# Kernel tuning notes

Hardware: AMD Instinct MI355X
Metric: run time of the kernel (lower is better)

## Reference

```python
import jax, jax.numpy as jnp
import numpy as np

O = 100000   # num objects
R = 1000000  # num triplets
D = 128      # per-slot feature dim (input_dim[0]=input_dim[1]=input_dim[2])
SUM_D = 3 * D  # MLP in/out width
H = 256      # hidden_dim


def setup_inputs() -> dict:
    key = jax.random.key(0)
    k1, k2, k3, k4, k5 = jax.random.split(key, 5)
    object_feats = jax.random.normal(k1, (O, D), dtype=jnp.float32)
    relation_feats = jax.random.normal(k2, (R, D), dtype=jnp.float32)
    triplet = jax.random.randint(k3, (R, 3), 0, O, dtype=jnp.int64)
    # MLP: Linear(SUM_D->H) + ReLU + Linear(H->SUM_D), kaiming-normal init
    W1 = jax.random.normal(k4, (SUM_D, H), dtype=jnp.float32) * np.sqrt(2.0 / SUM_D)
    b1 = jnp.zeros((H,), dtype=jnp.float32)
    W2 = jax.random.normal(k5, (H, SUM_D), dtype=jnp.float32) * np.sqrt(2.0 / H)
    b2 = jnp.zeros((SUM_D,), dtype=jnp.float32)
    return {
        "object_feats": object_feats,
        "relation_feats": relation_feats,
        "W1": W1, "b1": b1, "W2": W2, "b2": b2,
        "triplet": triplet,
        "triplet_len": R,
    }


def reference(object_feats, relation_feats, W1, b1, W2, b2, triplet, triplet_len):
    t = triplet[:triplet_len]                      # [R, 3]
    subs = t[:, 0]                                 # [R]
    objs = t[:, 1]                                 # [R]
    # gather subj/obj feats, concat with relation feats -> [R, 3D]
    gcn_feat = jnp.concatenate(
        [object_feats[subs], relation_feats, object_feats[objs]], axis=1)
    # 2-layer MLP
    h = jax.nn.relu(gcn_feat @ W1 + b1)            # [R, H]
    out = h @ W2 + b2                              # [R, 3D]
    sub_out = out[:, :D]
    rel_out = out[:, D:-D]
    obj_out = out[:, -D:]
    # scatter-add back to object nodes, then mean by degree, plus residual
    acc = jnp.zeros_like(object_feats)
    acc = acc.at[subs].add(sub_out).at[objs].add(obj_out)   # [O, D]
    one = jnp.ones((triplet_len,), dtype=object_feats.dtype)
    cnt = jnp.zeros((object_feats.shape[0],), dtype=object_feats.dtype)
    cnt = cnt.at[subs].add(one).at[objs].add(one)           # [O]
    output_feat = acc / jnp.clip(cnt, 1.0)[:, None] + object_feats
    return (output_feat, rel_out, triplet, triplet_len)
```

## Files before the change

### kernel.cpp

```cpp
#include <hip/hip_runtime.h>

#define O_N 100000
#define R_N 1000000
#define DIM 128
#define SD 384
#define HD 256
#define BR 64
#define OBJ8 (O_N * DIM / 8)
#define REL8 (R_N * DIM / 8)

typedef __attribute__((ext_vector_type(8))) short short8;
typedef __attribute__((ext_vector_type(4))) float f32x4;

static __device__ __forceinline__ unsigned short f2bf(float x) {
    union { float f; unsigned int u; } v; v.f = x;
    unsigned int r = v.u + 0x7FFFu + ((v.u >> 16) & 1u);
    return (unsigned short)(r >> 16);
}
static __device__ __forceinline__ unsigned long long pack4(f32x4 v) {
    return  (unsigned long long)f2bf(v.x)
         | ((unsigned long long)f2bf(v.y) << 16)
         | ((unsigned long long)f2bf(v.z) << 32)
         | ((unsigned long long)f2bf(v.w) << 48);
}

__global__ void prep_weights(const float* __restrict__ W1, const float* __restrict__ W2,
                             unsigned short* __restrict__ W1T, unsigned short* __restrict__ W2T) {
    int i = blockIdx.x * 256 + threadIdx.x;
    if (i < SD * HD) {
        int h = i / SD, k = i - h * SD;
        W1T[i] = f2bf(W1[k * HD + h]);
    } else {
        int j = i - SD * HD;
        int c = j / HD, k = j - c * HD;
        W2T[j] = f2bf(W2[k * SD + c]);
    }
}

__global__ void conv_bf16(const float* __restrict__ objF, const float* __restrict__ relF,
                          unsigned short* __restrict__ objBF, unsigned short* __restrict__ relBF) {
    long long i = (long long)blockIdx.x * 256 + threadIdx.x;
    if (i >= (long long)OBJ8 + REL8) return;
    const float* s; unsigned short* d;
    if (i < OBJ8) { s = objF + i * 8;           d = objBF + i * 8; }
    else          { long long j = i - OBJ8; s = relF + j * 8; d = relBF + j * 8; }
    f32x4 v0 = ((const f32x4*)s)[0];
    f32x4 v1 = ((const f32x4*)s)[1];
    unsigned long long* dd = (unsigned long long*)d;
    dd[0] = pack4(v0);
    dd[1] = pack4(v1);
}

__global__ void trip_cnt(const int* __restrict__ trip, float* __restrict__ tripOut,
                         float* __restrict__ lenOut, float* __restrict__ cnt,
                         const int* __restrict__ tlen) {
    int i = blockIdx.x * 256 + threadIdx.x;
    if (i < R_N) {
        int s = trip[3 * i], o = trip[3 * i + 1], t2 = trip[3 * i + 2];
        tripOut[3 * i]     = (float)s;
        tripOut[3 * i + 1] = (float)o;
        tripOut[3 * i + 2] = (float)t2;
        atomicAdd(&cnt[min(max(s, 0), O_N - 1)], 1.0f);
        atomicAdd(&cnt[min(max(o, 0), O_N - 1)], 1.0f);
        if (i == 0) lenOut[0] = (float)tlen[0];
    }
}

__global__ __launch_bounds__(256, 3)
void mlp_kernel(const unsigned short* __restrict__ objBF, const unsigned short* __restrict__ relBF,
                const unsigned short* __restrict__ W1T, const unsigned short* __restrict__ W2T,
                const float* __restrict__ b1, const float* __restrict__ b2,
                const int* __restrict__ trip,
                float* __restrict__ accB, float* __restrict__ relOut) {
    __shared__ __align__(16) unsigned char smem[49664];
    unsigned char* Xs = smem;
    unsigned char* Hs = smem;
    int* idxBuf = (int*)(smem + 49152);

    const int tid  = threadIdx.x;
    const int lane = tid & 63;
    const int w    = tid >> 6;
    const int r0   = blockIdx.x * BR;
    const int l15  = lane & 15;
    const int l4   = lane >> 4;

    if (tid < 2 * BR) {
        int rr = r0 + (tid & (BR - 1));
        int which = tid >> 6;
        idxBuf[tid] = min(max(trip[3 * rr + which], 0), O_N - 1);
    }
    __syncthreads();

    #pragma unroll
    for (int j = 0; j < 12; ++j) {
        int seg = w * 12 + j;
        int a   = seg * 64 + lane;
        int row = a / 48;
        int p   = a - row * 48;
        int u   = p ^ (row & 15);
        const unsigned short* src;
        if (u < 16)      src = objBF + (size_t)idxBuf[row] * DIM + u * 8;
        else if (u < 32) src = relBF + (size_t)(r0 + row) * DIM + (u - 16) * 8;
        else             src = objBF + (size_t)idxBuf[BR + row] * DIM + (u - 32) * 8;
        __builtin_amdgcn_global_load_lds(
            (const __attribute__((address_space(1))) void*)src,
            (__attribute__((address_space(3))) void*)(Xs + seg * 1024),
            16, 0, 0);
    }
    __syncthreads();

    const int hW = w * 64;
    f32x4 acc1[4][4];
    #pragma unroll
    for (int a = 0; a < 4; ++a)
        #pragma unroll
        for (int b = 0; b < 4; ++b) acc1[a][b] = (f32x4)0.0f;

    #pragma unroll
    for (int ks = 0; ks < 12; ++ks) {
        int k0 = ks * 32;
        short8 af[4], bfr[4];
        #pragma unroll
        for (int mh = 0; mh < 4; ++mh) {
            int h = hW + mh * 16 + l15;
            af[mh] = *(const short8*)(W1T + h * SD + k0 + 8 * l4);
        }
        #pragma unroll
        for (int nr = 0; nr < 4; ++nr) {
            int rel = nr * 16 + l15;
            int kb  = (k0 >> 3) + l4;
            bfr[nr] = *(const short8*)(Xs + rel * 768 + ((kb ^ (rel & 15)) << 4));
        }
        #pragma unroll
        for (int mh = 0; mh < 4; ++mh)
            #pragma unroll
            for (int nr = 0; nr < 4; ++nr)
                acc1[mh][nr] = __builtin_amdgcn_mfma_f32_16x16x32_bf16(
                    af[mh], bfr[nr], acc1[mh][nr], 0, 0, 0);
    }
    __syncthreads();

    #pragma unroll
    for (int mh = 0; mh < 4; ++mh) {
        int hbase = hW + mh * 16 + 4 * l4;
        float bb0 = b1[hbase], bb1 = b1[hbase + 1], bb2 = b1[hbase + 2], bb3 = b1[hbase + 3];
        int hb   = hbase >> 3;
        int half = (hbase >> 2) & 1;
        #pragma unroll
        for (int nr = 0; nr < 4; ++nr) {
            int rel = nr * 16 + l15;
            unsigned long long pk =
                  (unsigned long long)f2bf(fmaxf(acc1[mh][nr][0] + bb0, 0.f))
                | ((unsigned long long)f2bf(fmaxf(acc1[mh][nr][1] + bb1, 0.f)) << 16)
                | ((unsigned long long)f2bf(fmaxf(acc1[mh][nr][2] + bb2, 0.f)) << 32)
                | ((unsigned long long)f2bf(fmaxf(acc1[mh][nr][3] + bb3, 0.f)) << 48);
            *(unsigned long long*)(Hs + rel * 512 + ((hb ^ (rel & 15)) << 4) + half * 8) = pk;
        }
    }
    __syncthreads();

    const int cW = w * 96;
    f32x4 acc2[4][6];
    #pragma unroll
    for (int a = 0; a < 4; ++a)
        #pragma unroll
        for (int b = 0; b < 6; ++b) acc2[a][b] = (f32x4)0.0f;

    #pragma unroll
    for (int ks = 0; ks < 8; ++ks) {
        int k0 = ks * 32;
        short8 ha[4], wb[6];
        #pragma unroll
        for (int ma = 0; ma < 4; ++ma) {
            int rel = ma * 16 + l15;
            int hb  = (k0 >> 3) + l4;
            ha[ma] = *(const short8*)(Hs + rel * 512 + ((hb ^ (rel & 15)) << 4));
        }
        #pragma unroll
        for (int nb = 0; nb < 6; ++nb) {
            int c = cW + nb * 16 + l15;
            wb[nb] = *(const short8*)(W2T + c * HD + k0 + 8 * l4);
        }
        #pragma unroll
        for (int ma = 0; ma < 4; ++ma)
            #pragma unroll
            for (int nb = 0; nb < 6; ++nb)
                acc2[ma][nb] = __builtin_amdgcn_mfma_f32_16x16x32_bf16(
                    ha[ma], wb[nb], acc2[ma][nb], 0, 0, 0);
    }

    #pragma unroll
    for (int ma = 0; ma < 4; ++ma) {
        int rloc = ma * 16 + 4 * l4;
        int rg   = r0 + rloc;
        int subs[4], objs[4];
        #pragma unroll
        for (int q = 0; q < 4; ++q) {
            subs[q] = idxBuf[rloc + q];
            objs[q] = idxBuf[BR + rloc + q];
        }
        #pragma unroll
        for (int nb = 0; nb < 6; ++nb) {
            int c = cW + nb * 16 + l15;
            float b2v = b2[c];
            #pragma unroll
            for (int q = 0; q < 4; ++q) {
                float v = acc2[ma][nb][q] + b2v;
                if (c < DIM) {
                    atomicAdd(accB + (size_t)subs[q] * DIM + c, v);
                } else if (c < 2 * DIM) {
                    relOut[(size_t)(rg + q) * DIM + (c - DIM)] = v;
                } else {
                    atomicAdd(accB + (size_t)objs[q] * DIM + (c - 2 * DIM), v);
                }
            }
        }
    }
}

__global__ void finalize(const float* __restrict__ accB, const float* __restrict__ cnt,
                         const float* __restrict__ objF, float* __restrict__ outF) {
    int i = blockIdx.x * 256 + threadIdx.x;
    if (i < O_N * DIM / 4) {
        int row = i >> 5;
        float c = fmaxf(cnt[row], 1.0f);
        f32x4 a = ((const f32x4*)accB)[i];
        f32x4 o = ((const f32x4*)objF)[i];
        f32x4 r;
        r.x = a.x / c + o.x;
        r.y = a.y / c + o.y;
        r.z = a.z / c + o.z;
        r.w = a.w / c + o.w;
        ((f32x4*)outF)[i] = r;
    }
}

extern "C" void kernel_launch(void* const* d_in, const int* in_sizes, int n_in,
                              void* d_out, int out_size, void* d_ws, size_t ws_size,
                              hipStream_t stream) {
    const float* objF = (const float*)d_in[0];
    const float* relF = (const float*)d_in[1];
    const float* W1   = (const float*)d_in[2];
    const float* b1   = (const float*)d_in[3];
    const float* W2   = (const float*)d_in[4];
    const float* b2   = (const float*)d_in[5];
    const int*   trip = (const int*)d_in[6];
    const int*   tlen = (const int*)d_in[7];

    float* outF    = (float*)d_out;
    float* relOut  = outF + (size_t)O_N * DIM;
    float* tripOut = relOut + (size_t)R_N * DIM;
    float* lenOut  = tripOut + (size_t)R_N * 3;

    unsigned short* W1T = (unsigned short*)d_ws;
    unsigned short* W2T = W1T + SD * HD;
    float* accB = (float*)(W2T + SD * HD);
    float* cnt  = accB + (size_t)O_N * DIM;
    unsigned short* objBF = (unsigned short*)(cnt + O_N);
    unsigned short* relBF = objBF + (size_t)O_N * DIM;

    (void)hipMemsetAsync(accB, 0, ((size_t)O_N * DIM + O_N) * sizeof(float), stream);
    prep_weights<<<(2 * SD * HD) / 256, 256, 0, stream>>>(W1, W2, W1T, W2T);
    conv_bf16<<<(OBJ8 + REL8 + 255) / 256, 256, 0, stream>>>(objF, relF, objBF, relBF);
    trip_cnt<<<(R_N + 255) / 256, 256, 0, stream>>>(trip, tripOut, lenOut, cnt, tlen);
    mlp_kernel<<<R_N / BR, 256, 0, stream>>>(objBF, relBF, W1T, W2T, b1, b2, trip, accB, relOut);
    finalize<<<(O_N * DIM / 4 + 255) / 256, 256, 0, stream>>>(accB, cnt, objF, outF);
}
```

Before: 1.519 ms.

## Make MLP kernel persistent and prefetch next tile's gathered rows during compute

Converts the MLP kernel to a persistent grid of 512 blocks that loop over row tiles. It separates the X and H shared buffers so the next tile's gather into LDS can be issued while the second GEMM and the atomic scatter of the current tile run. The triplet kernel now writes clamped subject and object index arrays, so the MLP reads indices directly instead of staging them in LDS. This raises LDS use and lowers occupancy (launch bounds 3 to 2), and the hand-placed waitcnt and barrier synchronisation adds correctness risk.

```diff
diff --git a/kernel.cpp b/kernel.cpp
--- a/kernel.cpp
+++ b/kernel.cpp
@@ -6,11 +6,14 @@
 #define SD 384
 #define HD 256
 #define BR 64
+#define NT (R_N / BR)
+#define GRIDP 512
 #define OBJ8 (O_N * DIM / 8)
 #define REL8 (R_N * DIM / 8)
 
 typedef __attribute__((ext_vector_type(8))) short short8;
 typedef __attribute__((ext_vector_type(4))) float f32x4;
+typedef __attribute__((ext_vector_type(4))) int i32x4;
 
 static __device__ __forceinline__ unsigned short f2bf(float x) {
     union { float f; unsigned int u; } v; v.f = x;
@@ -53,6 +56,7 @@
 
 __global__ void trip_cnt(const int* __restrict__ trip, float* __restrict__ tripOut,
                          float* __restrict__ lenOut, float* __restrict__ cnt,
+                         int* __restrict__ subIdx, int* __restrict__ objIdx,
                          const int* __restrict__ tlen) {
     int i = blockIdx.x * 256 + threadIdx.x;
     if (i < R_N) {
@@ -60,162 +64,179 @@
         tripOut[3 * i]     = (float)s;
         tripOut[3 * i + 1] = (float)o;
         tripOut[3 * i + 2] = (float)t2;
-        atomicAdd(&cnt[min(max(s, 0), O_N - 1)], 1.0f);
-        atomicAdd(&cnt[min(max(o, 0), O_N - 1)], 1.0f);
+        int sc = min(max(s, 0), O_N - 1);
+        int oc = min(max(o, 0), O_N - 1);
+        subIdx[i] = sc;
+        objIdx[i] = oc;
+        atomicAdd(&cnt[sc], 1.0f);
+        atomicAdd(&cnt[oc], 1.0f);
         if (i == 0) lenOut[0] = (float)tlen[0];
     }
 }
 
-__global__ __launch_bounds__(256, 3)
+__global__ __launch_bounds__(256, 2)
 void mlp_kernel(const unsigned short* __restrict__ objBF, const unsigned short* __restrict__ relBF,
                 const unsigned short* __restrict__ W1T, const unsigned short* __restrict__ W2T,
                 const float* __restrict__ b1, const float* __restrict__ b2,
-                const int* __restrict__ trip,
+                const int* __restrict__ subIdx, const int* __restrict__ objIdx,
                 float* __restrict__ accB, float* __restrict__ relOut) {
-    __shared__ __align__(16) unsigned char smem[49664];
-    unsigned char* Xs = smem;
-    unsigned char* Hs = smem;
-    int* idxBuf = (int*)(smem + 49152);
+    __shared__ __align__(16) unsigned char Xs[49152];
+    __shared__ __align__(16) unsigned char Hs[32768];
 
     const int tid  = threadIdx.x;
     const int lane = tid & 63;
     const int w    = tid >> 6;
-    const int r0   = blockIdx.x * BR;
     const int l15  = lane & 15;
     const int l4   = lane >> 4;
-
-    if (tid < 2 * BR) {
-        int rr = r0 + (tid & (BR - 1));
-        int which = tid >> 6;
-        idxBuf[tid] = min(max(trip[3 * rr + which], 0), O_N - 1);
-    }
-    __syncthreads();
-
-    #pragma unroll
-    for (int j = 0; j < 12; ++j) {
-        int seg = w * 12 + j;
-        int a   = seg * 64 + lane;
-        int row = a / 48;
-        int p   = a - row * 48;
-        int u   = p ^ (row & 15);
-        const unsigned short* src;
-        if (u < 16)      src = objBF + (size_t)idxBuf[row] * DIM + u * 8;
-        else if (u < 32) src = relBF + (size_t)(r0 + row) * DIM + (u - 16) * 8;
-        else             src = objBF + (size_t)idxBuf[BR + row] * DIM + (u - 32) * 8;
-        __builtin_amdgcn_global_load_lds(
-            (const __attribute__((address_space(1))) void*)src,
-            (__attribute__((address_space(3))) void*)(Xs + seg * 1024),
-            16, 0, 0);
-    }
-    __syncthreads();
-
-    const int hW = w * 64;
-    f32x4 acc1[4][4];
-    #pragma unroll
-    for (int a = 0; a < 4; ++a)
-        #pragma unroll
-        for (int b = 0; b < 4; ++b) acc1[a][b] = (f32x4)0.0f;
-
-    #pragma unroll
-    for (int ks = 0; ks < 12; ++ks) {
-        int k0 = ks * 32;
-        short8 af[4], bfr[4];
+    const int hW   = w * 64;
+    const int cW   = w * 96;
+
+    #define FILL(TT)                                                          \
+    {                                                                         \
+        int rb_ = (TT) * BR;                                                  \
+        _Pragma("unroll")                                                     \
+        for (int j = 0; j < 12; ++j) {                                        \
+            int seg = w * 12 + j;                                             \
+            int a   = seg * 64 + lane;                                        \
+            int row = a / 48;                                                 \
+            int p   = a - row * 48;                                           \
+            int u   = p ^ (row & 15);                                         \
+            const unsigned short* src;                                        \
+            if (u < 16)      src = objBF + (size_t)subIdx[rb_ + row] * DIM + u * 8;        \
+            else if (u < 32) src = relBF + (size_t)(rb_ + row) * DIM + (u - 16) * 8;       \
+            else             src = objBF + (size_t)objIdx[rb_ + row] * DIM + (u - 32) * 8; \
+            __builtin_amdgcn_global_load_lds(                                 \
+                (const __attribute__((address_space(1))) void*)src,           \
+                (__attribute__((address_space(3))) void*)(Xs + seg * 1024),   \
+                16, 0, 0);                                                    \
+        }                                                                     \
+    }
+
+    int t = blockIdx.x;
+    if (t < NT) FILL(t);
+    asm volatile("s_waitcnt vmcnt(0)" ::: "memory");
+    __builtin_amdgcn_s_barrier();
+    __builtin_amdgcn_sched_barrier(0);
+
+    for (; t < NT; t += GRIDP) {
+        f32x4 acc1[4][4];
+        #pragma unroll
+        for (int a = 0; a < 4; ++a)
+            #pragma unroll
+            for (int b = 0; b < 4; ++b) acc1[a][b] = (f32x4)0.0f;
+
+        #pragma unroll
+        for (int ks = 0; ks < 12; ++ks) {
+            int k0 = ks * 32;
+            short8 af[4], bfr[4];
+            #pragma unroll
+            for (int mh = 0; mh < 4; ++mh) {
+                int h = hW + mh * 16 + l15;
+                af[mh] = *(const short8*)(W1T + h * SD + k0 + 8 * l4);
+            }
+            #pragma unroll
+            for (int nr = 0; nr < 4; ++nr) {
+                int rel = nr * 16 + l15;
+                int kb  = (k0 >> 3) + l4;
+                bfr[nr] = *(const short8*)(Xs + rel * 768 + ((kb ^ (rel & 15)) << 4));
+            }
+            #pragma unroll
+            for (int mh = 0; mh < 4; ++mh)
+                #pragma unroll
+                for (int nr = 0; nr < 4; ++nr)
+                    acc1[mh][nr] = __builtin_amdgcn_mfma_f32_16x16x32_bf16(
+                        af[mh], bfr[nr], acc1[mh][nr], 0, 0, 0);
+        }
+
+        __builtin_amdgcn_s_barrier();
+        __builtin_amdgcn_sched_barrier(0);
+
         #pragma unroll
         for (int mh = 0; mh < 4; ++mh) {
-            int h = hW + mh * 16 + l15;
-            af[mh] = *(const short8*)(W1T + h * SD + k0 + 8 * l4);
-        }
-        #pragma unroll
-        for (int nr = 0; nr < 4; ++nr) {
-            int rel = nr * 16 + l15;
-            int kb  = (k0 >> 3) + l4;
-            bfr[nr] = *(const short8*)(Xs + rel * 768 + ((kb ^ (rel & 15)) << 4));
-        }
-        #pragma unroll
-        for (int mh = 0; mh < 4; ++mh)
-            #pragma unroll
-            for (int nr = 0; nr < 4; ++nr)
-                acc1[mh][nr] = __builtin_amdgcn_mfma_f32_16x16x32_bf16(
-                    af[mh], bfr[nr], acc1[mh][nr], 0, 0, 0);
-    }
-    __syncthreads();
-
-    #pragma unroll
-    for (int mh = 0; mh < 4; ++mh) {
-        int hbase = hW + mh * 16 + 4 * l4;
-        float bb0 = b1[hbase], bb1 = b1[hbase + 1], bb2 = b1[hbase + 2], bb3 = b1[hbase + 3];
-        int hb   = hbase >> 3;
-        int half = (hbase >> 2) & 1;
-        #pragma unroll
-        for (int nr = 0; nr < 4; ++nr) {
-            int rel = nr * 16 + l15;
-            unsigned long long pk =
-                  (unsigned long long)f2bf(fmaxf(acc1[mh][nr][0] + bb0, 0.f))
-                | ((unsigned long long)f2bf(fmaxf(acc1[mh][nr][1] + bb1, 0.f)) << 16)
-                | ((unsigned long long)f2bf(fmaxf(acc1[mh][nr][2] + bb2, 0.f)) << 32)
-                | ((unsigned long long)f2bf(fmaxf(acc1[mh][nr][3] + bb3, 0.f)) << 48);
-            *(unsigned long long*)(Hs + rel * 512 + ((hb ^ (rel & 15)) << 4) + half * 8) = pk;
-        }
-    }
-    __syncthreads();
-
-    const int cW = w * 96;
-    f32x4 acc2[4][6];
-    #pragma unroll
-    for (int a = 0; a < 4; ++a)
-        #pragma unroll
-        for (int b = 0; b < 6; ++b) acc2[a][b] = (f32x4)0.0f;
-
-    #pragma unroll
-    for (int ks = 0; ks < 8; ++ks) {
-        int k0 = ks * 32;
-        short8 ha[4], wb[6];
-        #pragma unroll
-        for (int ma = 0; ma < 4; ++ma) {
-            int rel = ma * 16 + l15;
-            int hb  = (k0 >> 3) + l4;
-            ha[ma] = *(const short8*)(Hs + rel * 512 + ((hb ^ (rel & 15)) << 4));
-        }
-        #pragma unroll
-        for (int nb = 0; nb < 6; ++nb) {
-            int c = cW + nb * 16 + l15;
-            wb[nb] = *(const short8*)(W2T + c * HD + k0 + 8 * l4);
-        }
-        #pragma unroll
-        for (int ma = 0; ma < 4; ++ma)
-            #pragma unroll
-            for (int nb = 0; nb < 6; ++nb)
-                acc2[ma][nb] = __builtin_amdgcn_mfma_f32_16x16x32_bf16(
-                    ha[ma], wb[nb], acc2[ma][nb], 0, 0, 0);
-    }
-
-    #pragma unroll
-    for (int ma = 0; ma < 4; ++ma) {
-        int rloc = ma * 16 + 4 * l4;
-        int rg   = r0 + rloc;
-        int subs[4], objs[4];
-        #pragma unroll
-        for (int q = 0; q < 4; ++q) {
-            subs[q] = idxBuf[rloc + q];
-            objs[q] = idxBuf[BR + rloc + q];
-        }
-        #pragma unroll
-        for (int nb = 0; nb < 6; ++nb) {
-            int c = cW + nb * 16 + l15;
-            float b2v = b2[c];
-            #pragma unroll
-            for (int q = 0; q < 4; ++q) {
-                float v = acc2[ma][nb][q] + b2v;
-                if (c < DIM) {
-                    atomicAdd(accB + (size_t)subs[q] * DIM + c, v);
-                } else if (c < 2 * DIM) {
-                    relOut[(size_t)(rg + q) * DIM + (c - DIM)] = v;
-                } else {
-                    atomicAdd(accB + (size_t)objs[q] * DIM + (c - 2 * DIM), v);
+            int hbase = hW + mh * 16 + 4 * l4;
+            float bb0 = b1[hbase], bb1 = b1[hbase + 1], bb2 = b1[hbase + 2], bb3 = b1[hbase + 3];
+            int hb   = hbase >> 3;
+            int half = (hbase >> 2) & 1;
+            #pragma unroll
+            for (int nr = 0; nr < 4; ++nr) {
+                int rel = nr * 16 + l15;
+                unsigned long long pk =
+                      (unsigned long long)f2bf(fmaxf(acc1[mh][nr][0] + bb0, 0.f))
+                    | ((unsigned long long)f2bf(fmaxf(acc1[mh][nr][1] + bb1, 0.f)) << 16)
+                    | ((unsigned long long)f2bf(fmaxf(acc1[mh][nr][2] + bb2, 0.f)) << 32)
+                    | ((unsigned long long)f2bf(fmaxf(acc1[mh][nr][3] + bb3, 0.f)) << 48);
+                *(unsigned long long*)(Hs + rel * 512 + ((hb ^ (rel & 15)) << 4) + half * 8) = pk;
+            }
+        }
+        {
+            int tn = t + GRIDP;
+            if (tn < NT) FILL(tn);
+        }
+        asm volatile("s_waitcnt lgkmcnt(0)" ::: "memory");
+        __builtin_amdgcn_s_barrier();
+        __builtin_amdgcn_sched_barrier(0);
+
+        f32x4 acc2[4][6];
+        #pragma unroll
+        for (int a = 0; a < 4; ++a)
+            #pragma unroll
+            for (int b = 0; b < 6; ++b) acc2[a][b] = (f32x4)0.0f;
+
+        #pragma unroll
+        for (int ks = 0; ks < 8; ++ks) {
+            int k0 = ks * 32;
+            short8 ha[4], wb[6];
+            #pragma unroll
+            for (int ma = 0; ma < 4; ++ma) {
+                int rel = ma * 16 + l15;
+                int hb  = (k0 >> 3) + l4;
+                ha[ma] = *(const short8*)(Hs + rel * 512 + ((hb ^ (rel & 15)) << 4));
+            }
+            #pragma unroll
+            for (int nb = 0; nb < 6; ++nb) {
+                int c = cW + nb * 16 + l15;
+                wb[nb] = *(const short8*)(W2T + c * HD + k0 + 8 * l4);
+            }
+            #pragma unroll
+            for (int ma = 0; ma < 4; ++ma)
+                #pragma unroll
+                for (int nb = 0; nb < 6; ++nb)
+                    acc2[ma][nb] = __builtin_amdgcn_mfma_f32_16x16x32_bf16(
+                        ha[ma], wb[nb], acc2[ma][nb], 0, 0, 0);
+        }
+
+        asm volatile("s_waitcnt vmcnt(0)" ::: "memory");
+        __builtin_amdgcn_s_barrier();
+        __builtin_amdgcn_sched_barrier(0);
+
+        {
+            int r0t = t * BR;
+            #pragma unroll
+            for (int ma = 0; ma < 4; ++ma) {
+                int rloc = ma * 16 + 4 * l4;
+                int rg   = r0t + rloc;
+                i32x4 sv = *(const i32x4*)(subIdx + rg);
+                i32x4 ov = *(const i32x4*)(objIdx + rg);
+                #pragma unroll
+                for (int nb = 0; nb < 6; ++nb) {
+                    int c = cW + nb * 16 + l15;
+                    float b2v = b2[c];
+                    #pragma unroll
+                    for (int q = 0; q < 4; ++q) {
+                        float v = acc2[ma][nb][q] + b2v;
+                        if (c < DIM) {
+                            atomicAdd(accB + (size_t)sv[q] * DIM + c, v);
+                        } else if (c < 2 * DIM) {
+                            relOut[(size_t)(rg + q) * DIM + (c - DIM)] = v;
+                        } else {
+                            atomicAdd(accB + (size_t)ov[q] * DIM + (c - 2 * DIM), v);
+                        }
+                    }
                 }
             }
         }
     }
+    #undef FILL
 }
 
 __global__ void finalize(const float* __restrict__ accB, const float* __restrict__ cnt,
@@ -258,11 +279,13 @@
     float* cnt  = accB + (size_t)O_N * DIM;
     unsigned short* objBF = (unsigned short*)(cnt + O_N);
     unsigned short* relBF = objBF + (size_t)O_N * DIM;
+    int* subIdx = (int*)(relBF + (size_t)R_N * DIM);
+    int* objIdx = subIdx + R_N;
 
     (void)hipMemsetAsync(accB, 0, ((size_t)O_N * DIM + O_N) * sizeof(float), stream);
     prep_weights<<<(2 * SD * HD) / 256, 256, 0, stream>>>(W1, W2, W1T, W2T);
     conv_bf16<<<(OBJ8 + REL8 + 255) / 256, 256, 0, stream>>>(objF, relF, objBF, relBF);
-    trip_cnt<<<(R_N + 255) / 256, 256, 0, stream>>>(trip, tripOut, lenOut, cnt, tlen);
-    mlp_kernel<<<R_N / BR, 256, 0, stream>>>(objBF, relBF, W1T, W2T, b1, b2, trip, accB, relOut);
+    trip_cnt<<<(R_N + 255) / 256, 256, 0, stream>>>(trip, tripOut, lenOut, cnt, subIdx, objIdx, tlen);
+    mlp_kernel<<<GRIDP, 256, 0, stream>>>(objBF, relBF, W1T, W2T, b1, b2, subIdx, objIdx, accB, relOut);
     finalize<<<(O_N * DIM / 4 + 255) / 256, 256, 0, stream>>>(accB, cnt, objF, outF);
 }
```

After: 3.293 ms. 2.17x slower.

## Process two row tiles per block, prefetching the second tile during the epilogue

Applied to the files above, without the earlier changes.

Each block now handles two 64-row tiles, so half as many blocks are launched. After the second GEMM of the first tile, the block issues the asynchronous global-to-LDS gather for the second tile before running the atomic scatter epilogue, so the gather latency overlaps the epilogue. The second tile's indices are loaded while the first tile's hidden activations are being written. Halving the grid may reduce load balance and adds an extra barrier per tile.

```diff
diff --git a/kernel.cpp b/kernel.cpp
--- a/kernel.cpp
+++ b/kernel.cpp
@@ -6,6 +6,8 @@
 #define SD 384
 #define HD 256
 #define BR 64
+#define NT (R_N / BR)
+#define NB ((NT + 1) / 2)
 #define OBJ8 (O_N * DIM / 8)
 #define REL8 (R_N * DIM / 8)
 
@@ -72,150 +74,176 @@
                 const float* __restrict__ b1, const float* __restrict__ b2,
                 const int* __restrict__ trip,
                 float* __restrict__ accB, float* __restrict__ relOut) {
-    __shared__ __align__(16) unsigned char smem[49664];
+    __shared__ __align__(16) unsigned char smem[50176];
     unsigned char* Xs = smem;
     unsigned char* Hs = smem;
-    int* idxBuf = (int*)(smem + 49152);
+    int* idxA = (int*)(smem + 49152);
+    int* idxB = idxA + 128;
 
     const int tid  = threadIdx.x;
     const int lane = tid & 63;
     const int w    = tid >> 6;
-    const int r0   = blockIdx.x * BR;
     const int l15  = lane & 15;
     const int l4   = lane >> 4;
+    const int hW   = w * 64;
+    const int cW   = w * 96;
+
+    const int t1 = blockIdx.x;
+    const int t2 = blockIdx.x + NB;
+    const int hasT2 = (t2 < NT);
+
+    #define FILL(RB, IDXP)                                                    \
+    {                                                                         \
+        _Pragma("unroll")                                                     \
+        for (int j = 0; j < 12; ++j) {                                        \
+            int seg = w * 12 + j;                                             \
+            int a   = seg * 64 + lane;                                        \
+            int row = a / 48;                                                 \
+            int p   = a - row * 48;                                           \
+            int u   = p ^ (row & 15);                                         \
+            const unsigned short* src;                                        \
+            if (u < 16)      src = objBF + (size_t)(IDXP)[row] * DIM + u * 8;          \
+            else if (u < 32) src = relBF + (size_t)((RB) + row) * DIM + (u - 16) * 8;  \
+            else             src = objBF + (size_t)(IDXP)[BR + row] * DIM + (u - 32) * 8; \
+            __builtin_amdgcn_global_load_lds(                                 \
+                (const __attribute__((address_space(1))) void*)src,           \
+                (__attribute__((address_space(3))) void*)(Xs + seg * 1024),   \
+                16, 0, 0);                                                    \
+        }                                                                     \
+    }
 
     if (tid < 2 * BR) {
-        int rr = r0 + (tid & (BR - 1));
-        int which = tid >> 6;
-        idxBuf[tid] = min(max(trip[3 * rr + which], 0), O_N - 1);
+        int rr = t1 * BR + (tid & (BR - 1));
+        idxA[tid] = min(max(trip[3 * rr + (tid >> 6)], 0), O_N - 1);
     }
     __syncthreads();
-
-    #pragma unroll
-    for (int j = 0; j < 12; ++j) {
-        int seg = w * 12 + j;
-        int a   = seg * 64 + lane;
-        int row = a / 48;
-        int p   = a - row * 48;
-        int u   = p ^ (row & 15);
-        const unsigned short* src;
-        if (u < 16)      src = objBF + (size_t)idxBuf[row] * DIM + u * 8;
-        else if (u < 32) src = relBF + (size_t)(r0 + row) * DIM + (u - 16) * 8;
-        else             src = objBF + (size_t)idxBuf[BR + row] * DIM + (u - 32) * 8;
-        __builtin_amdgcn_global_load_lds(
-            (const __attribute__((address_space(1))) void*)src,
-            (__attribute__((address_space(3))) void*)(Xs + seg * 1024),
-            16, 0, 0);
-    }
-    __syncthreads();
-
-    const int hW = w * 64;
-    f32x4 acc1[4][4];
-    #pragma unroll
-    for (int a = 0; a < 4; ++a)
-        #pragma unroll
-        for (int b = 0; b < 4; ++b) acc1[a][b] = (f32x4)0.0f;
-
-    #pragma unroll
-    for (int ks = 0; ks < 12; ++ks) {
-        int k0 = ks * 32;
-        short8 af[4], bfr[4];
+    FILL(t1 * BR, idxA);
+
+    #pragma unroll 2
+    for (int s = 0; s < 2; ++s) {
+        if (s && !hasT2) break;
+        const int t = s ? t2 : t1;
+        const int* idxCur = s ? idxB : idxA;
+
+        __syncthreads();
+
+        f32x4 acc1[4][4];
+        #pragma unroll
+        for (int a = 0; a < 4; ++a)
+            #pragma unroll
+            for (int b = 0; b < 4; ++b) acc1[a][b] = (f32x4)0.0f;
+
+        #pragma unroll
+        for (int ks = 0; ks < 12; ++ks) {
+            int k0 = ks * 32;
+            short8 af[4], bfr[4];
+            #pragma unroll
+            for (int mh = 0; mh < 4; ++mh) {
+                int h = hW + mh * 16 + l15;
+                af[mh] = *(const short8*)(W1T + h * SD + k0 + 8 * l4);
+            }
+            #pragma unroll
+            for (int nr = 0; nr < 4; ++nr) {
+                int rel = nr * 16 + l15;
+                int kb  = (k0 >> 3) + l4;
+                bfr[nr] = *(const short8*)(Xs + rel * 768 + ((kb ^ (rel & 15)) << 4));
+            }
+            #pragma unroll
+            for (int mh = 0; mh < 4; ++mh)
+                #pragma unroll
+                for (int nr = 0; nr < 4; ++nr)
+                    acc1[mh][nr] = __builtin_amdgcn_mfma_f32_16x16x32_bf16(
+                        af[mh], bfr[nr], acc1[mh][nr], 0, 0, 0);
+        }
+        __syncthreads();
+
         #pragma unroll
         for (int mh = 0; mh < 4; ++mh) {
-            int h = hW + mh * 16 + l15;
-            af[mh] = *(const short8*)(W1T + h * SD + k0 + 8 * l4);
-        }
-        #pragma unroll
-        for (int nr = 0; nr < 4; ++nr) {
-            int rel = nr * 16 + l15;
-            int kb  = (k0 >> 3) + l4;
-            bfr[nr] = *(const short8*)(Xs + rel * 768 + ((kb ^ (rel & 15)) << 4));
-        }
-        #pragma unroll
-        for (int mh = 0; mh < 4; ++mh)
-            #pragma unroll
-            for (int nr = 0; nr < 4; ++nr)
-                acc1[mh][nr] = __builtin_amdgcn_mfma_f32_16x16x32_bf16(
-                    af[mh], bfr[nr], acc1[mh][nr], 0, 0, 0);
-    }
-    __syncthreads();
-
-    #pragma unroll
-    for (int mh = 0; mh < 4; ++mh) {
-        int hbase = hW + mh * 16 + 4 * l4;
-        float bb0 = b1[hbase], bb1 = b1[hbase + 1], bb2 = b1[hbase + 2], bb3 = b1[hbase + 3];
-        int hb   = hbase >> 3;
-        int half = (hbase >> 2) & 1;
-        #pragma unroll
-        for (int nr = 0; nr < 4; ++nr) {
-            int rel = nr * 16 + l15;
-            unsigned long long pk =
-                  (unsigned long long)f2bf(fmaxf(acc1[mh][nr][0] + bb0, 0.f))
-                | ((unsigned long long)f2bf(fmaxf(acc1[mh][nr][1] + bb1, 0.f)) << 16)
-                | ((unsigned long long)f2bf(fmaxf(acc1[mh][nr][2] + bb2, 0.f)) << 32)
-                | ((unsigned long long)f2bf(fmaxf(acc1[mh][nr][3] + bb3, 0.f)) << 48);
-            *(unsigned long long*)(Hs + rel * 512 + ((hb ^ (rel & 15)) << 4) + half * 8) = pk;
-        }
-    }
-    __syncthreads();
-
-    const int cW = w * 96;
-    f32x4 acc2[4][6];
-    #pragma unroll
-    for (int a = 0; a < 4; ++a)
-        #pragma unroll
-        for (int b = 0; b < 6; ++b) acc2[a][b] = (f32x4)0.0f;
-
-    #pragma unroll
-    for (int ks = 0; ks < 8; ++ks) {
-        int k0 = ks * 32;
-        short8 ha[4], wb[6];
-        #pragma unroll
-        for (int ma = 0; ma < 4; ++ma) {
-            int rel = ma * 16 + l15;
-            int hb  = (k0 >> 3) + l4;
-            ha[ma] = *(const short8*)(Hs + rel * 512 + ((hb ^ (rel & 15)) << 4));
-        }
-        #pragma unroll
-        for (int nb = 0; nb < 6; ++nb) {
-            int c = cW + nb * 16 + l15;
-            wb[nb] = *(const short8*)(W2T + c * HD + k0 + 8 * l4);
-        }
-        #pragma unroll
-        for (int ma = 0; ma < 4; ++ma)
-            #pragma unroll
-            for (int nb = 0; nb < 6; ++nb)
-                acc2[ma][nb] = __builtin_amdgcn_mfma_f32_16x16x32_bf16(
-                    ha[ma], wb[nb], acc2[ma][nb], 0, 0, 0);
-    }
-
-    #pragma unroll
-    for (int ma = 0; ma < 4; ++ma) {
-        int rloc = ma * 16 + 4 * l4;
-        int rg   = r0 + rloc;
-        int subs[4], objs[4];
-        #pragma unroll
-        for (int q = 0; q < 4; ++q) {
-            subs[q] = idxBuf[rloc + q];
-            objs[q] = idxBuf[BR + rloc + q];
-        }
-        #pragma unroll
-        for (int nb = 0; nb < 6; ++nb) {
-            int c = cW + nb * 16 + l15;
-            float b2v = b2[c];
-            #pragma unroll
-            for (int q = 0; q < 4; ++q) {
-                float v = acc2[ma][nb][q] + b2v;
-                if (c < DIM) {
-                    atomicAdd(accB + (size_t)subs[q] * DIM + c, v);
-                } else if (c < 2 * DIM) {
-                    relOut[(size_t)(rg + q) * DIM + (c - DIM)] = v;
-                } else {
-                    atomicAdd(accB + (size_t)objs[q] * DIM + (c - 2 * DIM), v);
+            int hbase = hW + mh * 16 + 4 * l4;
+            float bb0 = b1[hbase], bb1 = b1[hbase + 1], bb2 = b1[hbase + 2], bb3 = b1[hbase + 3];
+            int hb   = hbase >> 3;
+            int half = (hbase >> 2) & 1;
+            #pragma unroll
+            for (int nr = 0; nr < 4; ++nr) {
+                int rel = nr * 16 + l15;
+                unsigned long long pk =
+                      (unsigned long long)f2bf(fmaxf(acc1[mh][nr][0] + bb0, 0.f))
+                    | ((unsigned long long)f2bf(fmaxf(acc1[mh][nr][1] + bb1, 0.f)) << 16)
+                    | ((unsigned long long)f2bf(fmaxf(acc1[mh][nr][2] + bb2, 0.f)) << 32)
+                    | ((unsigned long long)f2bf(fmaxf(acc1[mh][nr][3] + bb3, 0.f)) << 48);
+                *(unsigned long long*)(Hs + rel * 512 + ((hb ^ (rel & 15)) << 4) + half * 8) = pk;
+            }
+        }
+        if (!s && hasT2 && tid < 2 * BR) {
+            int rr = t2 * BR + (tid & (BR - 1));
+            idxB[tid] = min(max(trip[3 * rr + (tid >> 6)], 0), O_N - 1);
+        }
+        __syncthreads();
+
+        f32x4 acc2[4][6];
+        #pragma unroll
+        for (int a = 0; a < 4; ++a)
+            #pragma unroll
+            for (int b = 0; b < 6; ++b) acc2[a][b] = (f32x4)0.0f;
+
+        #pragma unroll
+        for (int ks = 0; ks < 8; ++ks) {
+            int k0 = ks * 32;
+            short8 ha[4], wb[6];
+            #pragma unroll
+            for (int ma = 0; ma < 4; ++ma) {
+                int rel = ma * 16 + l15;
+                int hb  = (k0 >> 3) + l4;
+                ha[ma] = *(const short8*)(Hs + rel * 512 + ((hb ^ (rel & 15)) << 4));
+            }
+            #pragma unroll
+            for (int nb = 0; nb < 6; ++nb) {
+                int c = cW + nb * 16 + l15;
+                wb[nb] = *(const short8*)(W2T + c * HD + k0 + 8 * l4);
+            }
+            #pragma unroll
+            for (int ma = 0; ma < 4; ++ma)
+                #pragma unroll
+                for (int nb = 0; nb < 6; ++nb)
+                    acc2[ma][nb] = __builtin_amdgcn_mfma_f32_16x16x32_bf16(
+                        ha[ma], wb[nb], acc2[ma][nb], 0, 0, 0);
+        }
+        __syncthreads();
+
+        if (!s && hasT2) FILL(t2 * BR, idxB);
+
+        {
+            int r0t = t * BR;
+            #pragma unroll
+            for (int ma = 0; ma < 4; ++ma) {
+                int rloc = ma * 16 + 4 * l4;
+                int rg   = r0t + rloc;
+                int subs[4], objs[4];
+                #pragma unroll
+                for (int q = 0; q < 4; ++q) {
+                    subs[q] = idxCur[rloc + q];
+                    objs[q] = idxCur[BR + rloc + q];
                 }
-            }
-        }
-    }
+                #pragma unroll
+                for (int nb = 0; nb < 6; ++nb) {
+                    int c = cW + nb * 16 + l15;
+                    float b2v = b2[c];
+                    #pragma unroll
+                    for (int q = 0; q < 4; ++q) {
+                        float v = acc2[ma][nb][q] + b2v;
+                        if (c < DIM) {
+                            atomicAdd(accB + (size_t)subs[q] * DIM + c, v);
+                        } else if (c < 2 * DIM) {
+                            relOut[(size_t)(rg + q) * DIM + (c - DIM)] = v;
+                        } else {
+                            atomicAdd(accB + (size_t)objs[q] * DIM + (c - 2 * DIM), v);
+                        }
+                    }
+                }
+            }
+        }
+    }
+    #undef FILL
 }
 
 __global__ void finalize(const float* __restrict__ accB, const float* __restrict__ cnt,
@@ -263,6 +291,6 @@
     prep_weights<<<(2 * SD * HD) / 256, 256, 0, stream>>>(W1, W2, W1T, W2T);
     conv_bf16<<<(OBJ8 + REL8 + 255) / 256, 256, 0, stream>>>(objF, relF, objBF, relBF);
     trip_cnt<<<(R_N + 255) / 256, 256, 0, stream>>>(trip, tripOut, lenOut, cnt, tlen);
-    mlp_kernel<<<R_N / BR, 256, 0, stream>>>(objBF, relBF, W1T, W2T, b1, b2, trip, accB, relOut);
+    mlp_kernel<<<NB, 256, 0, stream>>>(objBF, relBF, W1T, W2T, b1, b2, trip, accB, relOut);
     finalize<<<(O_N * DIM / 4 + 255) / 256, 256, 0, stream>>>(accB, cnt, objF, outF);
 }
```

Measured after the change: 1.942 ms. 1.28x slower.
